# Kernel optimization log

Measured on AMD Instinct MI355X. Metric: run time of the kernel, lower is better.

The kernel has to match this reference:

```python
import jax, jax.numpy as jnp
import numpy as np

N_HEADS = 8
EPS = 1e-12  # F.normalize eps


def setup_inputs() -> dict:
    key = jax.random.key(0)
    ks = jax.random.split(key, 7)
    B, M, S, D = 2, 4, 2048, 512
    scale = 1.0 / np.sqrt(D)
    return {
        "x": jax.random.normal(ks[0], (B, M, S, D), dtype=jnp.float32),
        "Wq": jax.random.normal(ks[1], (D, D), dtype=jnp.float32) * scale,
        "bq": jax.random.normal(ks[2], (D,), dtype=jnp.float32) * 0.01,
        "Wkv": jax.random.normal(ks[3], (D, D), dtype=jnp.float32) * scale,
        "bkv": jax.random.normal(ks[4], (D,), dtype=jnp.float32) * 0.01,
        "Wo": jax.random.normal(ks[5], (D, D), dtype=jnp.float32) * scale,
        "bo": jax.random.normal(ks[6], (D,), dtype=jnp.float32) * 0.01,
    }


def _heads(t, H):
    # [B,M,S,D] -> [B,M,H,S,dk]
    B, Mo, S, D = t.shape
    return t.reshape(B, Mo, S, H, D // H).swapaxes(2, 3)


def reference(x, Wq, bq, Wkv, bkv, Wo, bo):
    B, Mo, S, D = x.shape
    H = N_HEADS
    # nn.Linear: y = x @ W^T + b
    Q = x @ Wq.T + bq
    KV = x @ Wkv.T + bkv  # K and V share this projection
    Qh = _heads(Q, H)
    Kh = _heads(KV, H)
    Vh = Kh
    # L2-normalize along head dim (cosine attention)
    Qn = Qh / jnp.maximum(jnp.linalg.norm(Qh, axis=-1, keepdims=True), EPS)
    Kn = Kh / jnp.maximum(jnp.linalg.norm(Kh, axis=-1, keepdims=True), EPS)
    scores = jnp.einsum("bmhqd,bmhkd->bmhqk", Qn, Kn)
    attn = jax.nn.softmax(scores, axis=-1)  # dropout=0 (eval)
    ctx = jnp.einsum("bmhqk,bmhkd->bmhqd", attn, Vh)
    ctx = ctx.swapaxes(2, 3).reshape(B, Mo, S, D)
    return ctx @ Wo.T + bo
```

## Files before the change

### kernel.cpp

```cpp
#include <hip/hip_runtime.h>

typedef __attribute__((ext_vector_type(8))) short bf16x8;
typedef __attribute__((ext_vector_type(8))) _Float16 f16x8;
typedef __attribute__((ext_vector_type(2))) _Float16 f16x2;
typedef __attribute__((ext_vector_type(4))) float f32x4;
typedef __attribute__((ext_vector_type(16))) float f32x16;
typedef __attribute__((ext_vector_type(2))) unsigned int u32x2;

__device__ __forceinline__ unsigned short f2bf(float f) {
  union { float f; unsigned int i; } v;
  v.f = f;
  unsigned int r = v.i + 0x7FFFu + ((v.i >> 16) & 1u);
  return (unsigned short)(r >> 16);
}

__device__ __forceinline__ f16x2 cvt_pk(float a, float b) {
  return __builtin_bit_cast(f16x2, __builtin_amdgcn_cvt_pkrtz(a, b));
}

__device__ __forceinline__ unsigned as_u32(f16x2 x) {
  return __builtin_bit_cast(unsigned int, x);
}
__device__ __forceinline__ f16x2 as_f16x2(unsigned x) {
  return __builtin_bit_cast(f16x2, x);
}

#if __has_builtin(__builtin_amdgcn_permlane32_swap)
__device__ __forceinline__ u32x2 plswap(unsigned a, unsigned b) {
  return __builtin_amdgcn_permlane32_swap(a, b, false, false);
}
#else
__device__ __forceinline__ u32x2 plswap(unsigned a, unsigned b) {
  unsigned pa = (unsigned)__shfl_xor((int)a, 32);
  unsigned pb = (unsigned)__shfl_xor((int)b, 32);
  int hi = (int)(threadIdx.x & 32);
  u32x2 r;
  r.x = hi ? pb : a;
  r.y = hi ? b : pa;
  return r;
}
#endif

__device__ __forceinline__ f16x8 pack4(f16x2 a, f16x2 b, f16x2 c, f16x2 d) {
  union { f16x2 h[4]; f16x8 v; } u;
  u.h[0] = a; u.h[1] = b; u.h[2] = c; u.h[3] = d;
  return u.v;
}

__device__ __forceinline__ void gl_lds16(const unsigned short* g, unsigned short* l) {
  __builtin_amdgcn_global_load_lds(
      (const __attribute__((address_space(1))) unsigned int*)g,
      (__attribute__((address_space(3))) unsigned int*)l, 16, 0, 0);
}

__device__ __forceinline__ f16x2 exp_poly(f16x2 x) {
  const f16x2 a5 = {(_Float16)0.00868682f, (_Float16)0.00868682f};
  const f16x2 a4 = {(_Float16)0.04379392f, (_Float16)0.04379392f};
  const f16x2 a3 = {(_Float16)0.16648887f, (_Float16)0.16648887f};
  const f16x2 a2 = {(_Float16)0.49919676f, (_Float16)0.49919676f};
  const f16x2 a1 = {(_Float16)1.00002229f, (_Float16)1.00002229f};
  const f16x2 a0 = {(_Float16)1.00004478f, (_Float16)1.00004478f};
#if __has_builtin(__builtin_elementwise_fma)
  f16x2 r = a5;
  r = __builtin_elementwise_fma(r, x, a4);
  r = __builtin_elementwise_fma(r, x, a3);
  r = __builtin_elementwise_fma(r, x, a2);
  r = __builtin_elementwise_fma(r, x, a1);
  r = __builtin_elementwise_fma(r, x, a0);
#else
  f16x2 r = a5;
  r = r * x + a4;
  r = r * x + a3;
  r = r * x + a2;
  r = r * x + a1;
  r = r * x + a0;
#endif
  return r;
}

__device__ __forceinline__ float dot2acc(f16x2 a, float acc) {
#if __has_builtin(__builtin_amdgcn_fdot2)
  const f16x2 one2 = {(_Float16)1.0f, (_Float16)1.0f};
  return __builtin_amdgcn_fdot2(a, one2, acc, false);
#else
  return acc + (float)a.x + (float)a.y;
#endif
}

__global__ __launch_bounds__(256) void cvt_all(
    const float* __restrict__ x, const float* __restrict__ wq,
    const float* __restrict__ wkv, const float* __restrict__ wo,
    unsigned short* __restrict__ xf, unsigned short* __restrict__ wqf,
    unsigned short* __restrict__ wkvf, unsigned short* __restrict__ wof) {
  int b = blockIdx.x;
  const float* in;
  unsigned short* out;
  int i;
  if (b < 8192) { in = x; out = xf; i = b * 256 + threadIdx.x; }
  else if (b < 8448) { in = wq; out = wqf; i = (b - 8192) * 256 + threadIdx.x; }
  else if (b < 8704) { in = wkv; out = wkvf; i = (b - 8448) * 256 + threadIdx.x; }
  else { in = wo; out = wof; i = (b - 8704) * 256 + threadIdx.x; }
  float4 v = ((const float4*)in)[i];
  int f = i << 2;
  int row = f >> 9, c = f & 511;
  long off = ((((long)(row >> 7) * 8 + (c >> 6)) * 16 + ((row >> 4) & 7) * 2 +
               ((c >> 5) & 1)) * 64 + ((c >> 3) & 3) * 16 + (row & 15)) * 8 + (c & 7);
  ushort4 o;
  o.x = f2bf(v.x);
  o.y = f2bf(v.y);
  o.z = f2bf(v.z);
  o.w = f2bf(v.w);
  *(ushort4*)(out + off) = o;
}

__global__ __launch_bounds__(256) void gemm_qkv(
    const unsigned short* __restrict__ xf, const unsigned short* __restrict__ Wqf,
    const unsigned short* __restrict__ Wkvf, const float* __restrict__ bq,
    const float* __restrict__ bkv, unsigned short* __restrict__ Qn,
    unsigned short* __restrict__ Kf, unsigned short* __restrict__ Vf) {
  __shared__ __attribute__((aligned(16))) unsigned short lA[16 * 512];
  __shared__ __attribute__((aligned(16))) unsigned short lB[16 * 512];
  const int isKV = (int)(blockIdx.y >> 2);
  const unsigned short* Btf = isKV ? Wkvf : Wqf;
  const float* bias = isKV ? bkv : bq;
  const int tid = threadIdx.x;
  const int lane = tid & 63;
  const int quad = lane >> 4, m16 = lane & 15;
  const int w = tid >> 6;
  const int wm = w >> 1, wn = w & 1;
  const long mb = (long)blockIdx.x * 128;
  const int nt = (int)(blockIdx.y & 3);
  const long nb = (long)nt * 128;
  f32x4 acc[4][4];
#pragma unroll
  for (int i = 0; i < 4; i++)
#pragma unroll
    for (int j = 0; j < 4; j++) acc[i][j] = (f32x4){0.f, 0.f, 0.f, 0.f};

  for (int kb = 0; kb < 8; kb++) {
    __syncthreads();
    {
      const unsigned short* gA =
          xf + (((long)blockIdx.x * 8 + kb) * 16 + 4 * w) * 512 + lane * 8;
      gl_lds16(gA, &lA[(4 * w + 0) * 512]);
      gl_lds16(gA + 512, &lA[(4 * w + 1) * 512]);
      gl_lds16(gA + 1024, &lA[(4 * w + 2) * 512]);
      gl_lds16(gA + 1536, &lA[(4 * w + 3) * 512]);
      const unsigned short* gB =
          Btf + (((long)nt * 8 + kb) * 16 + 4 * w) * 512 + lane * 8;
      gl_lds16(gB, &lB[(4 * w + 0) * 512]);
      gl_lds16(gB + 512, &lB[(4 * w + 1) * 512]);
      gl_lds16(gB + 1024, &lB[(4 * w + 2) * 512]);
      gl_lds16(gB + 1536, &lB[(4 * w + 3) * 512]);
    }
    __syncthreads();
#pragma unroll
    for (int ks = 0; ks < 2; ks++) {
      bf16x8 af[4], bfr[4];
#pragma unroll
      for (int i = 0; i < 4; i++)
        af[i] = *(const bf16x8*)&lA[(((wm * 4 + i) << 1) | ks) * 512 + lane * 8];
#pragma unroll
      for (int j = 0; j < 4; j++)
        bfr[j] = *(const bf16x8*)&lB[(((wn * 4 + j) << 1) | ks) * 512 + lane * 8];
#pragma unroll
      for (int i = 0; i < 4; i++)
#pragma unroll
        for (int j = 0; j < 4; j++)
          acc[i][j] =
              __builtin_amdgcn_mfma_f32_16x16x32_bf16(af[i], bfr[j], acc[i][j], 0, 0, 0);
    }
  }
  const int h = (int)(nb >> 6) + wn;
#pragma unroll
  for (int i = 0; i < 4; i++) {
    long row0 = mb + wm * 64 + i * 16 + quad * 4;
    float bb[4], val[4][4], inv[4];
#pragma unroll
    for (int j = 0; j < 4; j++) {
      bb[j] = bias[nb + wn * 64 + j * 16 + m16];
#pragma unroll
      for (int r = 0; r < 4; r++) val[j][r] = acc[i][j][r] + bb[j];
    }
#pragma unroll
    for (int r = 0; r < 4; r++) {
      float s = val[0][r] * val[0][r] + val[1][r] * val[1][r] +
                val[2][r] * val[2][r] + val[3][r] * val[3][r];
      s += __shfl_xor(s, 1);
      s += __shfl_xor(s, 2);
      s += __shfl_xor(s, 4);
      s += __shfl_xor(s, 8);
      inv[r] = 1.0f / fmaxf(sqrtf(s), 1e-12f);
    }
    if (!isKV) {
#pragma unroll
      for (int r = 0; r < 4; r++)
#pragma unroll
        for (int j = 0; j < 4; j++) {
          long col = nb + wn * 64 + j * 16 + m16;
          Qn[(row0 + r) * 512 + col] = f2bf(val[j][r] * inv[r]);
        }
    } else {
      const int bm2 = (int)(row0 >> 11);
      const int gq = bm2 * 8 + h;
      const int kt = (int)((row0 & 2047) >> 6);
      const long tb = ((long)gq * 32 + kt) * 8;
#pragma unroll
      for (int j = 0; j < 4; j++) {
        long kb0 = (tb + (i >> 1) * 4 + j) * 512 +
                   ((((i & 1) * 16 + quad * 4) | ((m16 >> 3) << 5)) * 8) + (m16 & 7);
#pragma unroll
        for (int r = 0; r < 4; r++) Kf[kb0 + r * 8] = f2bf(val[j][r] * inv[r]);
      }
#pragma unroll
      for (int j = 0; j < 4; j++) {
        long vo = (tb + (j >> 1) * 4 + i) * 512 +
                  ((((j & 1) * 16 + m16) | ((quad >> 1) << 5)) * 8) + (quad & 1) * 4;
        f16x2 lo = cvt_pk(val[j][0], val[j][1]);
        f16x2 hi2 = cvt_pk(val[j][2], val[j][3]);
        uint2 pk = make_uint2(__builtin_bit_cast(unsigned int, lo),
                              __builtin_bit_cast(unsigned int, hi2));
        *(uint2*)(Vf + vo) = pk;
      }
    }
  }
}

__global__ __launch_bounds__(256) void gemm_o(
    const unsigned short* __restrict__ Af, const unsigned short* __restrict__ Btf,
    const float* __restrict__ bias, float* __restrict__ Cout) {
  __shared__ __attribute__((aligned(16))) unsigned short lA[16 * 512];
  __shared__ __attribute__((aligned(16))) unsigned short lB[16 * 512];
  const int tid = threadIdx.x;
  const int lane = tid & 63;
  const int quad = lane >> 4, m16 = lane & 15;
  const int w = tid >> 6;
  const int wm = w >> 1, wn = w & 1;
  const long mb = (long)blockIdx.x * 128;
  const int nt = (int)blockIdx.y;
  const long nb = (long)nt * 128;
  f32x4 acc[4][4];
#pragma unroll
  for (int i = 0; i < 4; i++)
#pragma unroll
    for (int j = 0; j < 4; j++) acc[i][j] = (f32x4){0.f, 0.f, 0.f, 0.f};

  for (int kb = 0; kb < 8; kb++) {
    __syncthreads();
    {
      const unsigned short* gA =
          Af + (((long)blockIdx.x * 8 + kb) * 16 + 4 * w) * 512 + lane * 8;
      gl_lds16(gA, &lA[(4 * w + 0) * 512]);
      gl_lds16(gA + 512, &lA[(4 * w + 1) * 512]);
      gl_lds16(gA + 1024, &lA[(4 * w + 2) * 512]);
      gl_lds16(gA + 1536, &lA[(4 * w + 3) * 512]);
      const unsigned short* gB =
          Btf + (((long)nt * 8 + kb) * 16 + 4 * w) * 512 + lane * 8;
      gl_lds16(gB, &lB[(4 * w + 0) * 512]);
      gl_lds16(gB + 512, &lB[(4 * w + 1) * 512]);
      gl_lds16(gB + 1024, &lB[(4 * w + 2) * 512]);
      gl_lds16(gB + 1536, &lB[(4 * w + 3) * 512]);
    }
    __syncthreads();
#pragma unroll
    for (int ks = 0; ks < 2; ks++) {
      bf16x8 af[4], bfr[4];
#pragma unroll
      for (int i = 0; i < 4; i++)
        af[i] = *(const bf16x8*)&lA[(((wm * 4 + i) << 1) | ks) * 512 + lane * 8];
#pragma unroll
      for (int j = 0; j < 4; j++)
        bfr[j] = *(const bf16x8*)&lB[(((wn * 4 + j) << 1) | ks) * 512 + lane * 8];
#pragma unroll
      for (int i = 0; i < 4; i++)
#pragma unroll
        for (int j = 0; j < 4; j++)
          acc[i][j] =
              __builtin_amdgcn_mfma_f32_16x16x32_bf16(af[i], bfr[j], acc[i][j], 0, 0, 0);
    }
  }
#pragma unroll
  for (int i = 0; i < 4; i++) {
    long row0 = mb + wm * 64 + i * 16 + quad * 4;
#pragma unroll
    for (int j = 0; j < 4; j++) {
      long col = nb + wn * 64 + j * 16 + m16;
      float bb = bias[col];
#pragma unroll
      for (int r = 0; r < 4; r++) Cout[(row0 + r) * 512 + col] = acc[i][j][r] + bb;
    }
  }
}

__global__ __launch_bounds__(512, 4) void attn_cos(
    const unsigned short* __restrict__ Qn, const unsigned short* __restrict__ Kf,
    const unsigned short* __restrict__ Vf, unsigned short* __restrict__ ctxf) {
  __shared__ __attribute__((aligned(16))) unsigned short lK[2][8 * 512];
  __shared__ __attribute__((aligned(16))) unsigned short lVt[2][8 * 512];
  const int id = (int)blockIdx.x;
  const int g = ((id >> 6) << 3) | (id & 7);
  const int qt = (id >> 3) & 7;
  const int bm = g >> 3, h = g & 7;
  const int tid = threadIdx.x;
  const int lane = tid & 63;
  const int l31 = lane & 31, hi = lane >> 5;
  const int w = tid >> 6;
  const long qrow0 = (long)bm * 2048 + qt * 256 + w * 32;
  const int colbase = h * 64;

  bf16x8 qf[4];
#pragma unroll
  for (int dd = 0; dd < 4; dd++)
    qf[dd] = *(const bf16x8*)(Qn + (qrow0 + l31) * 512 + colbase + dd * 16 + hi * 8);

  f32x16 cacc[2];
#pragma unroll
  for (int e = 0; e < 16; e++) { cacc[0][e] = 0.f; cacc[1][e] = 0.f; }
  float lacc = 0.f;

  {
    const long tb0 = (long)g * 32 * 8;
    gl_lds16(Kf + (tb0 + w) * 512 + lane * 8, &lK[0][w * 512]);
    gl_lds16(Vf + (tb0 + w) * 512 + lane * 8, &lVt[0][w * 512]);
  }
  __syncthreads();

  int cur = 0;
  for (int kt = 0; kt < 32; ++kt) {
    {
      const int ktn = (kt + 1) & 31;
      const long tbn = ((long)g * 32 + ktn) * 8;
      gl_lds16(Kf + (tbn + w) * 512 + lane * 8, &lK[cur ^ 1][w * 512]);
      gl_lds16(Vf + (tbn + w) * 512 + lane * 8, &lVt[cur ^ 1][w * 512]);
    }

    f32x16 sacc[2];
#pragma unroll
    for (int e = 0; e < 16; e++) { sacc[0][e] = 0.f; sacc[1][e] = 0.f; }
#pragma unroll
    for (int dd = 0; dd < 4; dd++) {
      bf16x8 k0 = *(const bf16x8*)&lK[cur][(0 * 4 + dd) * 512 + lane * 8];
      bf16x8 k1 = *(const bf16x8*)&lK[cur][(1 * 4 + dd) * 512 + lane * 8];
      sacc[0] = __builtin_amdgcn_mfma_f32_32x32x16_bf16(k0, qf[dd], sacc[0], 0, 0, 0);
      sacc[1] = __builtin_amdgcn_mfma_f32_32x32x16_bf16(k1, qf[dd], sacc[1], 0, 0, 0);
    }

    f16x2 pe[2][8];
#pragma unroll
    for (int kk = 0; kk < 2; kk++)
#pragma unroll
      for (int t = 0; t < 8; t++) {
        f16x2 x = cvt_pk(sacc[kk][2 * t], sacc[kk][2 * t + 1]);
        pe[kk][t] = exp_poly(x);
        lacc = dot2acc(pe[kk][t], lacc);
      }

#pragma unroll
    for (int kk = 0; kk < 2; kk++)
#pragma unroll
      for (int s = 0; s < 2; s++) {
        u32x2 r0 = plswap(as_u32(pe[kk][4 * s + 0]), as_u32(pe[kk][4 * s + 2]));
        u32x2 r1 = plswap(as_u32(pe[kk][4 * s + 1]), as_u32(pe[kk][4 * s + 3]));
        f16x8 pa = pack4(as_f16x2(r0.x), as_f16x2(r1.x), as_f16x2(r0.y), as_f16x2(r1.y));
        const int ksub = kk * 2 + s;
        f16x8 v0 = *(const f16x8*)&lVt[cur][(0 * 4 + ksub) * 512 + lane * 8];
        f16x8 v1 = *(const f16x8*)&lVt[cur][(1 * 4 + ksub) * 512 + lane * 8];
        cacc[0] = __builtin_amdgcn_mfma_f32_32x32x16_f16(pa, v0, cacc[0], 0, 0, 0);
        cacc[1] = __builtin_amdgcn_mfma_f32_32x32x16_f16(pa, v1, cacc[1], 0, 0, 0);
      }

    __syncthreads();
    cur ^= 1;
  }

  lacc += __shfl_xor(lacc, 32);
  float linv[16];
#pragma unroll
  for (int r = 0; r < 16; r++) {
    int qr = (r & 3) + 8 * (r >> 2) + 4 * hi;
    linv[r] = 1.0f / __shfl(lacc, qr);
  }

#pragma unroll
  for (int dt = 0; dt < 2; dt++) {
    const int c = colbase + dt * 32 + l31;
    const long ckb = (long)(c >> 6);
    const int cbit = (c >> 5) & 1;
    const int lane16 = ((c >> 3) & 3) * 16;
    const int e = c & 7;
#pragma unroll
    for (int r = 0; r < 16; r++) {
      long row = qrow0 + (r & 3) + 8 * (r >> 2) + 4 * hi;
      long off = ((((row >> 7) * 8 + ckb) * 16 + ((row >> 4) & 7) * 2 + cbit) * 64 +
                  lane16 + (row & 15)) * 8 + e;
      ctxf[off] = f2bf(cacc[dt][r] * linv[r]);
    }
  }
}

extern "C" void kernel_launch(void* const* d_in, const int* in_sizes, int n_in,
                              void* d_out, int out_size, void* d_ws, size_t ws_size,
                              hipStream_t stream) {
  (void)in_sizes; (void)n_in; (void)out_size; (void)ws_size;
  const float* x = (const float*)d_in[0];
  const float* Wq = (const float*)d_in[1];
  const float* bq = (const float*)d_in[2];
  const float* Wkv = (const float*)d_in[3];
  const float* bkv = (const float*)d_in[4];
  const float* Wo = (const float*)d_in[5];
  const float* bo = (const float*)d_in[6];

  char* ws = (char*)d_ws;
  unsigned short* xf     = (unsigned short*)(ws);
  unsigned short* Wqf    = (unsigned short*)(ws + 16777216);
  unsigned short* Wkvf   = (unsigned short*)(ws + 17301504);
  unsigned short* Wof    = (unsigned short*)(ws + 17825792);
  unsigned short* Qn_bf  = (unsigned short*)(ws + 18350080);
  unsigned short* Kf     = (unsigned short*)(ws + 35127296);
  unsigned short* Vf     = (unsigned short*)(ws + 51904512);
  unsigned short* ctxf   = xf;

  cvt_all<<<8960, 256, 0, stream>>>(x, Wq, Wkv, Wo, xf, Wqf, Wkvf, Wof);

  gemm_qkv<<<dim3(128, 8), 256, 0, stream>>>(xf, Wqf, Wkvf, bq, bkv, Qn_bf, Kf, Vf);

  attn_cos<<<512, 512, 0, stream>>>(Qn_bf, Kf, Vf, ctxf);

  gemm_o<<<dim3(128, 4), 256, 0, stream>>>(ctxf, Wof, bo, (float*)d_out);
}
```

Baseline: 229.6 us.

## Triple-buffer K/V LDS tiles with partial vmcnt waits and MFMA priority hints

Switches the attention kernel's K/V shared-memory staging from double to triple buffering, prefetching two tiles ahead. The full __syncthreads is replaced by a waitcnt that leaves the newest two loads in flight, plus a raw s_barrier. s_setprio is raised around the MFMA sections. The goal is to hide global-to-LDS latency and reduce barrier stalls, at the cost of 50% more LDS per block, which may reduce occupancy at 4 blocks per CU.

```diff
diff --git a/kernel.cpp b/kernel.cpp
--- a/kernel.cpp
+++ b/kernel.cpp
@@ -295,8 +295,8 @@
 __global__ __launch_bounds__(512, 4) void attn_cos(
     const unsigned short* __restrict__ Qn, const unsigned short* __restrict__ Kf,
     const unsigned short* __restrict__ Vf, unsigned short* __restrict__ ctxf) {
-  __shared__ __attribute__((aligned(16))) unsigned short lK[2][8 * 512];
-  __shared__ __attribute__((aligned(16))) unsigned short lVt[2][8 * 512];
+  __shared__ __attribute__((aligned(16))) unsigned short lK[3][8 * 512];
+  __shared__ __attribute__((aligned(16))) unsigned short lVt[3][8 * 512];
   const int id = (int)blockIdx.x;
   const int g = ((id >> 6) << 3) | (id & 7);
   const int qt = (id >> 3) & 7;
@@ -318,32 +318,38 @@
   for (int e = 0; e < 16; e++) { cacc[0][e] = 0.f; cacc[1][e] = 0.f; }
   float lacc = 0.f;
 
-  {
-    const long tb0 = (long)g * 32 * 8;
-    gl_lds16(Kf + (tb0 + w) * 512 + lane * 8, &lK[0][w * 512]);
-    gl_lds16(Vf + (tb0 + w) * 512 + lane * 8, &lVt[0][w * 512]);
-  }
-  __syncthreads();
-
-  int cur = 0;
+#define STAGE(buf, ktn)                                                  \
+  {                                                                      \
+    const long tb_ = ((long)g * 32 + (ktn)) * 8;                         \
+    gl_lds16(Kf + (tb_ + w) * 512 + lane * 8, &lK[(buf)][w * 512]);      \
+    gl_lds16(Vf + (tb_ + w) * 512 + lane * 8, &lVt[(buf)][w * 512]);     \
+  }
+
+  STAGE(0, 0);
+  STAGE(1, 1);
+  asm volatile("s_waitcnt vmcnt(2)" ::: "memory");
+  __builtin_amdgcn_s_barrier();
+  __builtin_amdgcn_sched_barrier(0);
+
+  int cur = 0, nxt = 2;
   for (int kt = 0; kt < 32; ++kt) {
-    {
-      const int ktn = (kt + 1) & 31;
-      const long tbn = ((long)g * 32 + ktn) * 8;
-      gl_lds16(Kf + (tbn + w) * 512 + lane * 8, &lK[cur ^ 1][w * 512]);
-      gl_lds16(Vf + (tbn + w) * 512 + lane * 8, &lVt[cur ^ 1][w * 512]);
-    }
+    STAGE(nxt, (kt + 2) & 31);
+    __builtin_amdgcn_sched_barrier(0);
+    const unsigned short* bK = lK[cur];
+    const unsigned short* bV = lVt[cur];
 
     f32x16 sacc[2];
 #pragma unroll
     for (int e = 0; e < 16; e++) { sacc[0][e] = 0.f; sacc[1][e] = 0.f; }
+    __builtin_amdgcn_s_setprio(1);
 #pragma unroll
     for (int dd = 0; dd < 4; dd++) {
-      bf16x8 k0 = *(const bf16x8*)&lK[cur][(0 * 4 + dd) * 512 + lane * 8];
-      bf16x8 k1 = *(const bf16x8*)&lK[cur][(1 * 4 + dd) * 512 + lane * 8];
+      bf16x8 k0 = *(const bf16x8*)&bK[(0 * 4 + dd) * 512 + lane * 8];
+      bf16x8 k1 = *(const bf16x8*)&bK[(1 * 4 + dd) * 512 + lane * 8];
       sacc[0] = __builtin_amdgcn_mfma_f32_32x32x16_bf16(k0, qf[dd], sacc[0], 0, 0, 0);
       sacc[1] = __builtin_amdgcn_mfma_f32_32x32x16_bf16(k1, qf[dd], sacc[1], 0, 0, 0);
     }
+    __builtin_amdgcn_s_setprio(0);
 
     f16x2 pe[2][8];
 #pragma unroll
@@ -355,6 +361,7 @@
         lacc = dot2acc(pe[kk][t], lacc);
       }
 
+    __builtin_amdgcn_s_setprio(1);
 #pragma unroll
     for (int kk = 0; kk < 2; kk++)
 #pragma unroll
@@ -363,15 +370,21 @@
         u32x2 r1 = plswap(as_u32(pe[kk][4 * s + 1]), as_u32(pe[kk][4 * s + 3]));
         f16x8 pa = pack4(as_f16x2(r0.x), as_f16x2(r1.x), as_f16x2(r0.y), as_f16x2(r1.y));
         const int ksub = kk * 2 + s;
-        f16x8 v0 = *(const f16x8*)&lVt[cur][(0 * 4 + ksub) * 512 + lane * 8];
-        f16x8 v1 = *(const f16x8*)&lVt[cur][(1 * 4 + ksub) * 512 + lane * 8];
+        f16x8 v0 = *(const f16x8*)&bV[(0 * 4 + ksub) * 512 + lane * 8];
+        f16x8 v1 = *(const f16x8*)&bV[(1 * 4 + ksub) * 512 + lane * 8];
         cacc[0] = __builtin_amdgcn_mfma_f32_32x32x16_f16(pa, v0, cacc[0], 0, 0, 0);
         cacc[1] = __builtin_amdgcn_mfma_f32_32x32x16_f16(pa, v1, cacc[1], 0, 0, 0);
       }
-
-    __syncthreads();
-    cur ^= 1;
-  }
+    __builtin_amdgcn_s_setprio(0);
+
+    asm volatile("s_waitcnt vmcnt(2) lgkmcnt(0)" ::: "memory");
+    __builtin_amdgcn_sched_barrier(0);
+    __builtin_amdgcn_s_barrier();
+    __builtin_amdgcn_sched_barrier(0);
+    cur = (cur == 2) ? 0 : cur + 1;
+    nxt = (nxt == 2) ? 0 : nxt + 1;
+  }
+#undef STAGE
 
   lacc += __shfl_xor(lacc, 32);
   float linv[16];
```

After: 230.3 us. No clear change (+0.3%).

## Read K/V fragments straight from global in attention and compute row sums with MFMA

Applied to the files above, without the earlier changes.

The attention kernel no longer stages K/V tiles through double-buffered LDS with per-iteration barriers. Each wave now loads its K and V fragments directly from global memory (relying on L2/L1 for reuse) and processes the two 32-key halves one at a time to cut register pressure. The softmax denominator comes from an extra MFMA against a ones vector instead of dot2 accumulation plus cross-lane shuffles. Blocks shrink to 256 threads covering 128 query rows, with twice as many blocks. The trade is more global/L2 traffic, since K/V are no longer shared through LDS across waves, plus extra MFMA work for the sums.

```diff
diff --git a/kernel.cpp b/kernel.cpp
--- a/kernel.cpp
+++ b/kernel.cpp
@@ -76,15 +76,6 @@
   r = r * x + a0;
 #endif
   return r;
-}
-
-__device__ __forceinline__ float dot2acc(f16x2 a, float acc) {
-#if __has_builtin(__builtin_amdgcn_fdot2)
-  const f16x2 one2 = {(_Float16)1.0f, (_Float16)1.0f};
-  return __builtin_amdgcn_fdot2(a, one2, acc, false);
-#else
-  return acc + (float)a.x + (float)a.y;
-#endif
 }
 
 __global__ __launch_bounds__(256) void cvt_all(
@@ -292,20 +283,18 @@
   }
 }
 
-__global__ __launch_bounds__(512, 4) void attn_cos(
+__global__ __launch_bounds__(256, 3) void attn_cos(
     const unsigned short* __restrict__ Qn, const unsigned short* __restrict__ Kf,
     const unsigned short* __restrict__ Vf, unsigned short* __restrict__ ctxf) {
-  __shared__ __attribute__((aligned(16))) unsigned short lK[2][8 * 512];
-  __shared__ __attribute__((aligned(16))) unsigned short lVt[2][8 * 512];
   const int id = (int)blockIdx.x;
-  const int g = ((id >> 6) << 3) | (id & 7);
-  const int qt = (id >> 3) & 7;
+  const int g = ((id >> 7) << 3) | (id & 7);
+  const int qt = (id >> 3) & 15;
   const int bm = g >> 3, h = g & 7;
   const int tid = threadIdx.x;
   const int lane = tid & 63;
   const int l31 = lane & 31, hi = lane >> 5;
   const int w = tid >> 6;
-  const long qrow0 = (long)bm * 2048 + qt * 256 + w * 32;
+  const long qrow0 = (long)bm * 2048 + qt * 128 + w * 32;
   const int colbase = h * 64;
 
   bf16x8 qf[4];
@@ -314,72 +303,57 @@
     qf[dd] = *(const bf16x8*)(Qn + (qrow0 + l31) * 512 + colbase + dd * 16 + hi * 8);
 
   f32x16 cacc[2];
-#pragma unroll
-  for (int e = 0; e < 16; e++) { cacc[0][e] = 0.f; cacc[1][e] = 0.f; }
-  float lacc = 0.f;
-
-  {
-    const long tb0 = (long)g * 32 * 8;
-    gl_lds16(Kf + (tb0 + w) * 512 + lane * 8, &lK[0][w * 512]);
-    gl_lds16(Vf + (tb0 + w) * 512 + lane * 8, &lVt[0][w * 512]);
-  }
-  __syncthreads();
-
-  int cur = 0;
+  f32x16 caccl;
+#pragma unroll
+  for (int e = 0; e < 16; e++) { cacc[0][e] = 0.f; cacc[1][e] = 0.f; caccl[e] = 0.f; }
+  const f16x8 onesv = {(_Float16)1.0f, (_Float16)1.0f, (_Float16)1.0f, (_Float16)1.0f,
+                       (_Float16)1.0f, (_Float16)1.0f, (_Float16)1.0f, (_Float16)1.0f};
+  const f32x16 zv = {};
+
+  const unsigned short* baseK = Kf + ((long)g * 32) * 8 * 512 + lane * 8;
+  const unsigned short* baseV = Vf + ((long)g * 32) * 8 * 512 + lane * 8;
+
   for (int kt = 0; kt < 32; ++kt) {
-    {
-      const int ktn = (kt + 1) & 31;
-      const long tbn = ((long)g * 32 + ktn) * 8;
-      gl_lds16(Kf + (tbn + w) * 512 + lane * 8, &lK[cur ^ 1][w * 512]);
-      gl_lds16(Vf + (tbn + w) * 512 + lane * 8, &lVt[cur ^ 1][w * 512]);
-    }
-
-    f32x16 sacc[2];
-#pragma unroll
-    for (int e = 0; e < 16; e++) { sacc[0][e] = 0.f; sacc[1][e] = 0.f; }
-#pragma unroll
-    for (int dd = 0; dd < 4; dd++) {
-      bf16x8 k0 = *(const bf16x8*)&lK[cur][(0 * 4 + dd) * 512 + lane * 8];
-      bf16x8 k1 = *(const bf16x8*)&lK[cur][(1 * 4 + dd) * 512 + lane * 8];
-      sacc[0] = __builtin_amdgcn_mfma_f32_32x32x16_bf16(k0, qf[dd], sacc[0], 0, 0, 0);
-      sacc[1] = __builtin_amdgcn_mfma_f32_32x32x16_bf16(k1, qf[dd], sacc[1], 0, 0, 0);
-    }
-
-    f16x2 pe[2][8];
-#pragma unroll
-    for (int kk = 0; kk < 2; kk++)
-#pragma unroll
-      for (int t = 0; t < 8; t++) {
-        f16x2 x = cvt_pk(sacc[kk][2 * t], sacc[kk][2 * t + 1]);
-        pe[kk][t] = exp_poly(x);
-        lacc = dot2acc(pe[kk][t], lacc);
+    const unsigned short* pK = baseK + (long)kt * (8 * 512);
+    const unsigned short* pV = baseV + (long)kt * (8 * 512);
+#pragma unroll
+    for (int kk = 0; kk < 2; kk++) {
+      bf16x8 kf[4];
+      f16x8 vf[2][2];
+#pragma unroll
+      for (int dd = 0; dd < 4; dd++)
+        kf[dd] = *(const bf16x8*)(pK + (kk * 4 + dd) * 512);
+#pragma unroll
+      for (int s = 0; s < 2; s++)
+#pragma unroll
+        for (int dt = 0; dt < 2; dt++)
+          vf[s][dt] = *(const f16x8*)(pV + (dt * 4 + kk * 2 + s) * 512);
+
+      f32x16 sacc = __builtin_amdgcn_mfma_f32_32x32x16_bf16(kf[0], qf[0], zv, 0, 0, 0);
+#pragma unroll
+      for (int dd = 1; dd < 4; dd++)
+        sacc = __builtin_amdgcn_mfma_f32_32x32x16_bf16(kf[dd], qf[dd], sacc, 0, 0, 0);
+
+      f16x2 pe[8];
+#pragma unroll
+      for (int t = 0; t < 8; t++)
+        pe[t] = exp_poly(cvt_pk(sacc[2 * t], sacc[2 * t + 1]));
+
+#pragma unroll
+      for (int s = 0; s < 2; s++) {
+        u32x2 r0 = plswap(as_u32(pe[4 * s + 0]), as_u32(pe[4 * s + 2]));
+        u32x2 r1 = plswap(as_u32(pe[4 * s + 1]), as_u32(pe[4 * s + 3]));
+        f16x8 pa = pack4(as_f16x2(r0.x), as_f16x2(r1.x), as_f16x2(r0.y), as_f16x2(r1.y));
+        cacc[0] = __builtin_amdgcn_mfma_f32_32x32x16_f16(pa, vf[s][0], cacc[0], 0, 0, 0);
+        cacc[1] = __builtin_amdgcn_mfma_f32_32x32x16_f16(pa, vf[s][1], cacc[1], 0, 0, 0);
+        caccl = __builtin_amdgcn_mfma_f32_32x32x16_f16(pa, onesv, caccl, 0, 0, 0);
       }
-
-#pragma unroll
-    for (int kk = 0; kk < 2; kk++)
-#pragma unroll
-      for (int s = 0; s < 2; s++) {
-        u32x2 r0 = plswap(as_u32(pe[kk][4 * s + 0]), as_u32(pe[kk][4 * s + 2]));
-        u32x2 r1 = plswap(as_u32(pe[kk][4 * s + 1]), as_u32(pe[kk][4 * s + 3]));
-        f16x8 pa = pack4(as_f16x2(r0.x), as_f16x2(r1.x), as_f16x2(r0.y), as_f16x2(r1.y));
-        const int ksub = kk * 2 + s;
-        f16x8 v0 = *(const f16x8*)&lVt[cur][(0 * 4 + ksub) * 512 + lane * 8];
-        f16x8 v1 = *(const f16x8*)&lVt[cur][(1 * 4 + ksub) * 512 + lane * 8];
-        cacc[0] = __builtin_amdgcn_mfma_f32_32x32x16_f16(pa, v0, cacc[0], 0, 0, 0);
-        cacc[1] = __builtin_amdgcn_mfma_f32_32x32x16_f16(pa, v1, cacc[1], 0, 0, 0);
-      }
-
-    __syncthreads();
-    cur ^= 1;
-  }
-
-  lacc += __shfl_xor(lacc, 32);
+    }
+  }
+
   float linv[16];
 #pragma unroll
-  for (int r = 0; r < 16; r++) {
-    int qr = (r & 3) + 8 * (r >> 2) + 4 * hi;
-    linv[r] = 1.0f / __shfl(lacc, qr);
-  }
+  for (int r = 0; r < 16; r++) linv[r] = 1.0f / caccl[r];
 
 #pragma unroll
   for (int dt = 0; dt < 2; dt++) {
@@ -424,7 +398,7 @@
 
   gemm_qkv<<<dim3(128, 8), 256, 0, stream>>>(xf, Wqf, Wkvf, bq, bkv, Qn_bf, Kf, Vf);
 
-  attn_cos<<<512, 512, 0, stream>>>(Qn_bf, Kf, Vf, ctxf);
+  attn_cos<<<1024, 256, 0, stream>>>(Qn_bf, Kf, Vf, ctxf);
 
   gemm_o<<<dim3(128, 4), 256, 0, stream>>>(ctxf, Wof, bo, (float*)d_out);
 }
```

New measurement: 273.1 us. 19.0% more time.
